# Kernel tuning notes

Hardware: AMD Instinct MI355X
Metric: run time of the kernel (lower is better)

The kernel has to match this reference:

```python
import jax, jax.numpy as jnp
import numpy as np

EPS = 1e-5
H = 1024  # hidden_size
IN = 1024  # input_size
B = 4096


def _layer_norm(x, gamma, beta):
    mu = jnp.mean(x, axis=-1, keepdims=True)
    var = jnp.mean(jnp.square(x - mu), axis=-1, keepdims=True)
    return (x - mu) * jax.lax.rsqrt(var + EPS) * gamma + beta


def setup_inputs() -> dict:
    key = jax.random.key(0)
    ks = jax.random.split(key, 8)
    s_h = 1.0 / np.sqrt(H)
    s_x = 1.0 / np.sqrt(IN)
    return {
        "x": jax.random.normal(ks[0], (B, IN), dtype=jnp.float32),
        "h": jax.random.normal(ks[1], (B, H), dtype=jnp.float32),
        "c": jax.random.normal(ks[2], (B, H), dtype=jnp.float32),
        # hidden_lin: Linear(H, 4H) with bias; input_lin: Linear(IN, 4H) no bias
        "W_h": jax.random.uniform(ks[3], (H, 4 * H), jnp.float32, -s_h, s_h),
        "b_h": jax.random.uniform(ks[4], (4 * H,), jnp.float32, -s_h, s_h),
        "W_x": jax.random.uniform(ks[5], (IN, 4 * H), jnp.float32, -s_x, s_x),
        # 4 gate LayerNorms stacked [4,H], plus LayerNorm for c
        "ln_g": jnp.ones((4, H), jnp.float32),
        "ln_b": jnp.zeros((4, H), jnp.float32),
        "lnc_g": jnp.ones((H,), jnp.float32),
        "lnc_b": jnp.zeros((H,), jnp.float32),
    }


def reference(x, h, c, W_h, b_h, W_x, ln_g, ln_b, lnc_g, lnc_b):
    # ifgo = hidden_lin(h) + input_lin(x) : [B, 4H]
    ifgo = h @ W_h + b_h + x @ W_x
    ifgo = ifgo.reshape(x.shape[0], 4, H)  # [B, 4, H]
    ifgo = _layer_norm(ifgo, ln_g, ln_b)   # per-gate LayerNorm over last dim
    i, f, g, o = ifgo[:, 0], ifgo[:, 1], ifgo[:, 2], ifgo[:, 3]
    c_next = jax.nn.sigmoid(f) * c + jax.nn.sigmoid(i) * jnp.tanh(g)
    h_next = jax.nn.sigmoid(o) * jnp.tanh(_layer_norm(c_next, lnc_g, lnc_b))
    return (h_next, c_next)
```

## Files before the change

### kernel.cpp

```cpp
#include <hip/hip_runtime.h>

typedef short bf16x8 __attribute__((ext_vector_type(8)));
typedef unsigned short u16x8 __attribute__((ext_vector_type(8)));
typedef float f32x4  __attribute__((ext_vector_type(4)));

__device__ __forceinline__ float bf2f(unsigned short u) {
  union { unsigned int i; float f; } x; x.i = ((unsigned int)u) << 16; return x.f;
}
__device__ __forceinline__ unsigned short f2bf(float f) {
  union { float f; unsigned int i; } x; x.f = f;
  unsigned int r = x.i + 0x7fffu + ((x.i >> 16) & 1u);
  return (unsigned short)(r >> 16);
}
__device__ __forceinline__ float sigm(float v) { return 1.f / (1.f + __expf(-v)); }
__device__ __forceinline__ float tanh_(float v) { return 1.f - 2.f / (__expf(2.f * v) + 1.f); }
__device__ __forceinline__ int is_fp32(const void* lng) {
  return ((*(const unsigned int*)lng) & 0xFFFFu) == 0u;
}

#define AS1 __attribute__((address_space(1)))
#define AS3 __attribute__((address_space(3)))

__global__ __launch_bounds__(256) void prep_kernel(
    const void* __restrict__ h, const void* __restrict__ x,
    const void* __restrict__ Wh, const void* __restrict__ Wx,
    const void* __restrict__ lng,
    unsigned short* __restrict__ Ap, unsigned short* __restrict__ Wt)
{
  __shared__ __align__(16) unsigned short tkn[64][64];
  const int fp = is_fp32(lng);
  if (blockIdx.x < 4096) {
    const int row = blockIdx.x;
    const int col = threadIdx.x * 8;
    const void* src; int sc;
    if (col < 1024) { src = h; sc = col; } else { src = x; sc = col - 1024; }
    u16x8 o;
    if (fp) {
      const float* s = (const float*)src + (size_t)row * 1024 + sc;
      float4 a = *(const float4*)s;
      float4 b = *(const float4*)(s + 4);
      o[0] = f2bf(a.x); o[1] = f2bf(a.y); o[2] = f2bf(a.z); o[3] = f2bf(a.w);
      o[4] = f2bf(b.x); o[5] = f2bf(b.y); o[6] = f2bf(b.z); o[7] = f2bf(b.w);
    } else {
      o = *(const u16x8*)((const unsigned short*)src + (size_t)row * 1024 + sc);
    }
    *(u16x8*)(Ap + (size_t)row * 2048 + col) = o;
  } else {
    const int bid = blockIdx.x - 4096;
    const int n0 = (bid & 63) * 64;
    const int k0 = (bid >> 6) * 64;
    const int t = threadIdx.x;
    const void* src; int krow;
    if (k0 < 1024) { src = Wh; krow = k0; } else { src = Wx; krow = k0 - 1024; }
    if (fp) {
#pragma unroll
      for (int i = 0; i < 4; ++i) {
        const int k  = (t >> 4) + i * 16;
        const int n4 = (t & 15) * 4;
        float4 w = *(const float4*)((const float*)src + (size_t)(krow + k) * 4096 + n0 + n4);
        ushort4 u; u.x = f2bf(w.x); u.y = f2bf(w.y); u.z = f2bf(w.z); u.w = f2bf(w.w);
        *(ushort4*)&tkn[k][n4] = u;
      }
    } else {
#pragma unroll
      for (int i = 0; i < 2; ++i) {
        const int k  = (t >> 3) + i * 32;
        const int n8 = (t & 7) * 8;
        *(u16x8*)&tkn[k][n8] =
            *(const u16x8*)((const unsigned short*)src + (size_t)(krow + k) * 4096 + n0 + n8);
      }
    }
    __syncthreads();
#pragma unroll
    for (int i = 0; i < 2; ++i) {
      const int n  = (t >> 3) + i * 32;
      const int k8 = (t & 7) * 8;
      u16x8 o;
#pragma unroll
      for (int j = 0; j < 8; ++j) o[j] = tkn[k8 + j][n];
      *(u16x8*)(Wt + (size_t)(n0 + n) * 2048 + k0 + k8) = o;
    }
  }
}


#define BAR()   __builtin_amdgcn_s_barrier()
#define VMW(N)  { asm volatile("s_waitcnt vmcnt(" #N ")" ::: "memory"); }

#define LOAD_A(DB, MH)                                                         \
  { const unsigned short* _ba = &As[DB][(MH)*128 + wr*64 + fr][0];             \
    _Pragma("unroll") for (int mi = 0; mi < 4; ++mi)                           \
      _Pragma("unroll") for (int kh = 0; kh < 2; ++kh)                         \
        a[mi][kh] = *(const bf16x8*)(_ba + mi*1024 + ((kh*4 + fq) ^ xk) * 8); }

#define LOAD_B(DB, NH, BT)                                                     \
  { const unsigned short* _bb = &Bs[DB][(NH)*128 + wc*32 + fr][0];             \
    _Pragma("unroll") for (int ni = 0; ni < 2; ++ni)                           \
      _Pragma("unroll") for (int kh = 0; kh < 2; ++kh)                         \
        (BT)[ni][kh] = *(const bf16x8*)(_bb + ni*1024 + ((kh*4 + fq) ^ xk) * 8); }

#define MFMA16(MH, NH, BT)                                                     \
  { __builtin_amdgcn_s_setprio(1);                                             \
    _Pragma("unroll") for (int kh = 0; kh < 2; ++kh)                           \
      _Pragma("unroll") for (int mi = 0; mi < 4; ++mi)                         \
        _Pragma("unroll") for (int ni = 0; ni < 2; ++ni)                       \
          acc[MH][mi][NH][ni] = __builtin_amdgcn_mfma_f32_16x16x32_bf16(       \
              a[mi][kh], (BT)[ni][kh], acc[MH][mi][NH][ni], 0, 0, 0);          \
    __builtin_amdgcn_s_setprio(0); }

#define STAGE(G, LDS, ROW0, H, KT)                                             \
  { _Pragma("unroll") for (int l = 0; l < 2; ++l) {                            \
      const int _idx = l * 512 + tid;                                          \
      const int _r = _idx >> 3;                                                \
      const int _sg = (_idx & 7) ^ (_r & 7);                                   \
      const unsigned short* _src = (G) + (size_t)((ROW0) + (H)*128 + _r) * 2048\
                                   + ((KT) << 6) + _sg * 8;                    \
      __builtin_amdgcn_global_load_lds((const AS1 void*)_src,                  \
          (AS3 void*)(&(LDS)[0][0] + (H)*8192 + (l*512 + wave*64)*8), 16, 0, 0);\
  } }

__global__ __launch_bounds__(512, 2) void gemm_kernel(
    const unsigned short* __restrict__ Ap,
    const unsigned short* __restrict__ Wt,
    unsigned short* __restrict__ Cout)
{
  __shared__ __align__(16) unsigned short As[2][256][64];
  __shared__ __align__(16) unsigned short Bs[2][256][64];

  const int bid = blockIdx.x;
  const int swz = (bid & 7) * 32 + (bid >> 3);
  const int bm = swz >> 4, bn = swz & 15;
  const int arow = bm * 256, brow = bn * 256;

  const int tid  = threadIdx.x;
  const int wave = tid >> 6, lane = tid & 63;
  const int wr = wave >> 2, wc = wave & 3;
  const int fr = lane & 15, fq = lane >> 4;
  const int xk = fr & 7;

  f32x4 acc[2][4][2][2] = {};
  bf16x8 a[4][2], bA[2][2], bB[2][2];

  STAGE(Wt, Bs[0], brow, 0, 0);
  STAGE(Ap, As[0], arow, 0, 0);
  STAGE(Wt, Bs[0], brow, 1, 0);
  STAGE(Ap, As[0], arow, 1, 0);
  STAGE(Wt, Bs[1], brow, 0, 1);
  STAGE(Ap, As[1], arow, 0, 1);
  VMW(4);
  BAR();
  LOAD_B(0, 0, bA)

#pragma unroll 1
  for (int it = 0; it < 16; ++it) {
    const int t1 = (2 * it + 1) & 31;
    const int t2 = (2 * it + 2) & 31;
    const int t3 = (2 * it + 3) & 31;

    VMW(8);
    LOAD_A(0, 0)
    STAGE(Wt, Bs[1], brow, 1, t1);
    BAR();
    MFMA16(0, 0, bA);
    BAR();
    VMW(8);
    LOAD_B(0, 1, bB)
    STAGE(Ap, As[1], arow, 1, t1);
    BAR();
    MFMA16(0, 1, bB);
    BAR();
    VMW(8);
    LOAD_A(0, 1)
    STAGE(Wt, Bs[0], brow, 0, t2);
    BAR();
    MFMA16(1, 1, bB);
    BAR();
    VMW(8);
    LOAD_B(1, 0, bB)
    STAGE(Ap, As[0], arow, 0, t2);
    BAR();
    MFMA16(1, 0, bA);
    BAR();
    VMW(8);
    LOAD_A(1, 0)
    STAGE(Wt, Bs[0], brow, 1, t2);
    BAR();
    MFMA16(0, 0, bB);
    BAR();
    VMW(8);
    LOAD_B(1, 1, bA)
    STAGE(Ap, As[0], arow, 1, t2);
    BAR();
    MFMA16(0, 1, bA);
    BAR();
    VMW(8);
    LOAD_A(1, 1)
    STAGE(Wt, Bs[1], brow, 0, t3);
    BAR();
    MFMA16(1, 1, bA);
    BAR();
    VMW(8);
    LOAD_B(0, 0, bA)
    STAGE(Ap, As[1], arow, 0, t3);
    BAR();
    MFMA16(1, 0, bB);
    BAR();
  }
  VMW(0);

  unsigned short* Cb = Cout + (size_t)arow * 4096 + brow;
#pragma unroll
  for (int mh = 0; mh < 2; ++mh)
#pragma unroll
    for (int mi = 0; mi < 4; ++mi)
#pragma unroll
      for (int nh = 0; nh < 2; ++nh)
#pragma unroll
        for (int ni = 0; ni < 2; ++ni) {
          const int row = mh * 128 + wr * 64 + mi * 16 + fq * 4;
          const int col = nh * 128 + wc * 32 + ni * 16 + fr;
#pragma unroll
          for (int r = 0; r < 4; ++r)
            Cb[(size_t)(row + r) * 4096 + col] = f2bf(acc[mh][mi][nh][ni][r]);
        }
}

__device__ __forceinline__ float4 load4(const void* p, size_t idx, int fp) {
  if (fp) return *(const float4*)((const float*)p + idx);
  ushort4 u = *(const ushort4*)((const unsigned short*)p + idx);
  return make_float4(bf2f(u.x), bf2f(u.y), bf2f(u.z), bf2f(u.w));
}
__device__ __forceinline__ void store4(void* p, size_t idx, int fp,
                                       float a, float b, float c, float d) {
  if (fp) {
    *(float4*)((float*)p + idx) = make_float4(a, b, c, d);
  } else {
    ushort4 u; u.x = f2bf(a); u.y = f2bf(b); u.z = f2bf(c); u.w = f2bf(d);
    *(ushort4*)((unsigned short*)p + idx) = u;
  }
}

__global__ __launch_bounds__(256) void ln_lstm_kernel(
    const unsigned short* __restrict__ parts,
    const void* __restrict__ c,
    const void* __restrict__ bh,
    const void* __restrict__ ln_g,
    const void* __restrict__ ln_b,
    const void* __restrict__ lnc_g,
    const void* __restrict__ lnc_b,
    void* __restrict__ out)
{
  const int b = blockIdx.x;
  const int t = threadIdx.x;
  const int lane = t & 63, wave = t >> 6;
  const int fp = is_fp32(lnc_g);
  const unsigned short* P0 = parts + (size_t)b * 4096;

  __shared__ float sred[4][8];

  float v[4][4];
  float red[8];
#pragma unroll
  for (int q = 0; q < 4; ++q) {
    ushort4 p0 = *(const ushort4*)(P0 + q * 1024 + t * 4);
    float4 b4 = load4(bh, q * 1024 + t * 4, fp);
    v[q][0] = bf2f(p0.x) + b4.x;
    v[q][1] = bf2f(p0.y) + b4.y;
    v[q][2] = bf2f(p0.z) + b4.z;
    v[q][3] = bf2f(p0.w) + b4.w;
    red[q * 2]     = v[q][0] + v[q][1] + v[q][2] + v[q][3];
    red[q * 2 + 1] = v[q][0]*v[q][0] + v[q][1]*v[q][1] + v[q][2]*v[q][2] + v[q][3]*v[q][3];
  }
#pragma unroll
  for (int j = 0; j < 8; ++j) {
    float s = red[j];
#pragma unroll
    for (int off = 32; off > 0; off >>= 1) s += __shfl_down(s, off, 64);
    if (lane == 0) sred[wave][j] = s;
  }
  __syncthreads();
  float mu[4], rs[4];
#pragma unroll
  for (int q = 0; q < 4; ++q) {
    float s  = sred[0][2*q]   + sred[1][2*q]   + sred[2][2*q]   + sred[3][2*q];
    float sq = sred[0][2*q+1] + sred[1][2*q+1] + sred[2][2*q+1] + sred[3][2*q+1];
    mu[q] = s * (1.f / 1024.f);
    float var = sq * (1.f / 1024.f) - mu[q] * mu[q];
    rs[q] = rsqrtf(var + 1e-5f);
  }

  float4 gI = load4(ln_g, 0 * 1024 + t * 4, fp), bI = load4(ln_b, 0 * 1024 + t * 4, fp);
  float4 gF = load4(ln_g, 1 * 1024 + t * 4, fp), bF = load4(ln_b, 1 * 1024 + t * 4, fp);
  float4 gG = load4(ln_g, 2 * 1024 + t * 4, fp), bG = load4(ln_b, 2 * 1024 + t * 4, fp);
  float4 gO = load4(ln_g, 3 * 1024 + t * 4, fp), bO = load4(ln_b, 3 * 1024 + t * 4, fp);
  float gg[4][4] = { {gI.x,gI.y,gI.z,gI.w}, {gF.x,gF.y,gF.z,gF.w},
                     {gG.x,gG.y,gG.z,gG.w}, {gO.x,gO.y,gO.z,gO.w} };
  float gb[4][4] = { {bI.x,bI.y,bI.z,bI.w}, {bF.x,bF.y,bF.z,bF.w},
                     {bG.x,bG.y,bG.z,bG.w}, {bO.x,bO.y,bO.z,bO.w} };

  float4 c4 = load4(c, (size_t)b * 1024 + t * 4, fp);
  float cin[4] = { c4.x, c4.y, c4.z, c4.w };

  float cn[4], osg[4];
  float csum = 0.f, csq = 0.f;
#pragma unroll
  for (int e = 0; e < 4; ++e) {
    float iv = (v[0][e] - mu[0]) * rs[0] * gg[0][e] + gb[0][e];
    float fv = (v[1][e] - mu[1]) * rs[1] * gg[1][e] + gb[1][e];
    float gv = (v[2][e] - mu[2]) * rs[2] * gg[2][e] + gb[2][e];
    float ov = (v[3][e] - mu[3]) * rs[3] * gg[3][e] + gb[3][e];
    float cne = sigm(fv) * cin[e] + sigm(iv) * tanh_(gv);
    cn[e] = cne; csum += cne; csq += cne * cne;
    osg[e] = sigm(ov);
  }
  store4(out, (size_t)4096 * 1024 + (size_t)b * 1024 + t * 4, fp, cn[0], cn[1], cn[2], cn[3]);

  __syncthreads();
  {
    float s0 = csum, s1 = csq;
#pragma unroll
    for (int off = 32; off > 0; off >>= 1) { s0 += __shfl_down(s0, off, 64); s1 += __shfl_down(s1, off, 64); }
    if (lane == 0) { sred[wave][0] = s0; sred[wave][1] = s1; }
  }
  __syncthreads();
  float cs   = sred[0][0] + sred[1][0] + sred[2][0] + sred[3][0];
  float csq2 = sred[0][1] + sred[1][1] + sred[2][1] + sred[3][1];
  float mu_c = cs * (1.f / 1024.f);
  float var_c = csq2 * (1.f / 1024.f) - mu_c * mu_c;
  float rs_c = rsqrtf(var_c + 1e-5f);

  float4 cg4 = load4(lnc_g, t * 4, fp);
  float4 cb4 = load4(lnc_b, t * 4, fp);

  float hn[4];
  float cgv[4] = { cg4.x, cg4.y, cg4.z, cg4.w };
  float cbv[4] = { cb4.x, cb4.y, cb4.z, cb4.w };
#pragma unroll
  for (int e = 0; e < 4; ++e)
    hn[e] = osg[e] * tanh_((cn[e] - mu_c) * rs_c * cgv[e] + cbv[e]);
  store4(out, (size_t)b * 1024 + t * 4, fp, hn[0], hn[1], hn[2], hn[3]);
}

extern "C" void kernel_launch(void* const* d_in, const int* in_sizes, int n_in,
                              void* d_out, int out_size, void* d_ws, size_t ws_size,
                              hipStream_t stream) {
  const void* x    = d_in[0];
  const void* h    = d_in[1];
  const void* c    = d_in[2];
  const void* Wh   = d_in[3];
  const void* bh   = d_in[4];
  const void* Wx   = d_in[5];
  const void* lng  = d_in[6];
  const void* lnb  = d_in[7];
  const void* lncg = d_in[8];
  const void* lncb = d_in[9];

  char* ws = (char*)d_ws;
  unsigned short* parts = (unsigned short*)ws;
  unsigned short* Wt    = (unsigned short*)(ws + (size_t)64 * 1024 * 1024);
  unsigned short* Ap    = (unsigned short*)(ws + (size_t)80 * 1024 * 1024);

  prep_kernel<<<6144, 256, 0, stream>>>(h, x, Wh, Wx, lng, Ap, Wt);
  gemm_kernel<<<256, 512, 0, stream>>>(Ap, Wt, parts);
  ln_lstm_kernel<<<4096, 256, 0, stream>>>(parts, c, bh, lng, lnb, lncg, lncb, d_out);
}
```

Baseline: 219.9 us.

## Deepen GEMM LDS prefetch pipeline and process four rows per LN-LSTM block

The GEMM main loop now prefetches a full k-tile ahead, staging both halves of the next buffer in the prologue. It waits on vmcnt only twice per half-iteration instead of before every sub-step, with an explicit lgkmcnt wait before the barriers that flip buffers. This aims to hide global-load latency better and cut wait stalls, at the risk of subtle read/write races in the double-buffered LDS. Separately, the LN-LSTM epilogue kernel handles four batch rows per block, loading the gamma, beta and bias vectors once and reusing them, which reduces block count and redundant parameter loads.

```diff
diff --git a/kernel.cpp b/kernel.cpp
--- a/kernel.cpp
+++ b/kernel.cpp
@@ -86,6 +86,7 @@
 
 #define BAR()   __builtin_amdgcn_s_barrier()
 #define VMW(N)  { asm volatile("s_waitcnt vmcnt(" #N ")" ::: "memory"); }
+#define LGKM0() { asm volatile("s_waitcnt lgkmcnt(0)" ::: "memory"); }
 
 #define LOAD_A(DB, MH)                                                         \
   { const unsigned short* _ba = &As[DB][(MH)*128 + wr*64 + fr][0];             \
@@ -147,63 +148,61 @@
   STAGE(Ap, As[0], arow, 1, 0);
   STAGE(Wt, Bs[1], brow, 0, 1);
   STAGE(Ap, As[1], arow, 0, 1);
-  VMW(4);
+  STAGE(Wt, Bs[1], brow, 1, 1);
+  STAGE(Ap, As[1], arow, 1, 1);
+  VMW(8);
   BAR();
   LOAD_B(0, 0, bA)
+  LGKM0();
 
 #pragma unroll 1
   for (int it = 0; it < 16; ++it) {
-    const int t1 = (2 * it + 1) & 31;
     const int t2 = (2 * it + 2) & 31;
     const int t3 = (2 * it + 3) & 31;
 
-    VMW(8);
     LOAD_A(0, 0)
-    STAGE(Wt, Bs[1], brow, 1, t1);
+    STAGE(Wt, Bs[0], brow, 0, t2);
     BAR();
     MFMA16(0, 0, bA);
     BAR();
-    VMW(8);
     LOAD_B(0, 1, bB)
-    STAGE(Ap, As[1], arow, 1, t1);
+    STAGE(Ap, As[0], arow, 0, t2);
     BAR();
     MFMA16(0, 1, bB);
     BAR();
-    VMW(8);
     LOAD_A(0, 1)
-    STAGE(Wt, Bs[0], brow, 0, t2);
+    STAGE(Wt, Bs[0], brow, 1, t2);
     BAR();
     MFMA16(1, 1, bB);
     BAR();
-    VMW(8);
+    VMW(6);
     LOAD_B(1, 0, bB)
-    STAGE(Ap, As[0], arow, 0, t2);
+    STAGE(Ap, As[0], arow, 1, t2);
     BAR();
     MFMA16(1, 0, bA);
-    BAR();
-    VMW(8);
+    LGKM0();
+    BAR();
     LOAD_A(1, 0)
-    STAGE(Wt, Bs[0], brow, 1, t2);
+    STAGE(Wt, Bs[1], brow, 0, t3);
     BAR();
     MFMA16(0, 0, bB);
     BAR();
-    VMW(8);
     LOAD_B(1, 1, bA)
-    STAGE(Ap, As[0], arow, 1, t2);
+    STAGE(Ap, As[1], arow, 0, t3);
     BAR();
     MFMA16(0, 1, bA);
     BAR();
-    VMW(8);
     LOAD_A(1, 1)
-    STAGE(Wt, Bs[1], brow, 0, t3);
+    STAGE(Wt, Bs[1], brow, 1, t3);
     BAR();
     MFMA16(1, 1, bA);
     BAR();
-    VMW(8);
+    VMW(6);
     LOAD_B(0, 0, bA)
-    STAGE(Ap, As[1], arow, 0, t3);
+    STAGE(Ap, As[1], arow, 1, t3);
     BAR();
     MFMA16(1, 0, bB);
+    LGKM0();
     BAR();
   }
   VMW(0);
@@ -250,95 +249,101 @@
     const void* __restrict__ lnc_b,
     void* __restrict__ out)
 {
-  const int b = blockIdx.x;
   const int t = threadIdx.x;
   const int lane = t & 63, wave = t >> 6;
   const int fp = is_fp32(lnc_g);
-  const unsigned short* P0 = parts + (size_t)b * 4096;
 
   __shared__ float sred[4][8];
 
-  float v[4][4];
-  float red[8];
+  float4 bias4[4];
+#pragma unroll
+  for (int q = 0; q < 4; ++q) bias4[q] = load4(bh, q * 1024 + t * 4, fp);
+  float gg[4][4], gb[4][4];
 #pragma unroll
   for (int q = 0; q < 4; ++q) {
-    ushort4 p0 = *(const ushort4*)(P0 + q * 1024 + t * 4);
-    float4 b4 = load4(bh, q * 1024 + t * 4, fp);
-    v[q][0] = bf2f(p0.x) + b4.x;
-    v[q][1] = bf2f(p0.y) + b4.y;
-    v[q][2] = bf2f(p0.z) + b4.z;
-    v[q][3] = bf2f(p0.w) + b4.w;
-    red[q * 2]     = v[q][0] + v[q][1] + v[q][2] + v[q][3];
-    red[q * 2 + 1] = v[q][0]*v[q][0] + v[q][1]*v[q][1] + v[q][2]*v[q][2] + v[q][3]*v[q][3];
-  }
-#pragma unroll
-  for (int j = 0; j < 8; ++j) {
-    float s = red[j];
-#pragma unroll
-    for (int off = 32; off > 0; off >>= 1) s += __shfl_down(s, off, 64);
-    if (lane == 0) sred[wave][j] = s;
-  }
-  __syncthreads();
-  float mu[4], rs[4];
-#pragma unroll
-  for (int q = 0; q < 4; ++q) {
-    float s  = sred[0][2*q]   + sred[1][2*q]   + sred[2][2*q]   + sred[3][2*q];
-    float sq = sred[0][2*q+1] + sred[1][2*q+1] + sred[2][2*q+1] + sred[3][2*q+1];
-    mu[q] = s * (1.f / 1024.f);
-    float var = sq * (1.f / 1024.f) - mu[q] * mu[q];
-    rs[q] = rsqrtf(var + 1e-5f);
-  }
-
-  float4 gI = load4(ln_g, 0 * 1024 + t * 4, fp), bI = load4(ln_b, 0 * 1024 + t * 4, fp);
-  float4 gF = load4(ln_g, 1 * 1024 + t * 4, fp), bF = load4(ln_b, 1 * 1024 + t * 4, fp);
-  float4 gG = load4(ln_g, 2 * 1024 + t * 4, fp), bG = load4(ln_b, 2 * 1024 + t * 4, fp);
-  float4 gO = load4(ln_g, 3 * 1024 + t * 4, fp), bO = load4(ln_b, 3 * 1024 + t * 4, fp);
-  float gg[4][4] = { {gI.x,gI.y,gI.z,gI.w}, {gF.x,gF.y,gF.z,gF.w},
-                     {gG.x,gG.y,gG.z,gG.w}, {gO.x,gO.y,gO.z,gO.w} };
-  float gb[4][4] = { {bI.x,bI.y,bI.z,bI.w}, {bF.x,bF.y,bF.z,bF.w},
-                     {bG.x,bG.y,bG.z,bG.w}, {bO.x,bO.y,bO.z,bO.w} };
-
-  float4 c4 = load4(c, (size_t)b * 1024 + t * 4, fp);
-  float cin[4] = { c4.x, c4.y, c4.z, c4.w };
-
-  float cn[4], osg[4];
-  float csum = 0.f, csq = 0.f;
-#pragma unroll
-  for (int e = 0; e < 4; ++e) {
-    float iv = (v[0][e] - mu[0]) * rs[0] * gg[0][e] + gb[0][e];
-    float fv = (v[1][e] - mu[1]) * rs[1] * gg[1][e] + gb[1][e];
-    float gv = (v[2][e] - mu[2]) * rs[2] * gg[2][e] + gb[2][e];
-    float ov = (v[3][e] - mu[3]) * rs[3] * gg[3][e] + gb[3][e];
-    float cne = sigm(fv) * cin[e] + sigm(iv) * tanh_(gv);
-    cn[e] = cne; csum += cne; csq += cne * cne;
-    osg[e] = sigm(ov);
-  }
-  store4(out, (size_t)4096 * 1024 + (size_t)b * 1024 + t * 4, fp, cn[0], cn[1], cn[2], cn[3]);
-
-  __syncthreads();
-  {
-    float s0 = csum, s1 = csq;
-#pragma unroll
-    for (int off = 32; off > 0; off >>= 1) { s0 += __shfl_down(s0, off, 64); s1 += __shfl_down(s1, off, 64); }
-    if (lane == 0) { sred[wave][0] = s0; sred[wave][1] = s1; }
-  }
-  __syncthreads();
-  float cs   = sred[0][0] + sred[1][0] + sred[2][0] + sred[3][0];
-  float csq2 = sred[0][1] + sred[1][1] + sred[2][1] + sred[3][1];
-  float mu_c = cs * (1.f / 1024.f);
-  float var_c = csq2 * (1.f / 1024.f) - mu_c * mu_c;
-  float rs_c = rsqrtf(var_c + 1e-5f);
-
+    float4 g4 = load4(ln_g, q * 1024 + t * 4, fp);
+    float4 b4 = load4(ln_b, q * 1024 + t * 4, fp);
+    gg[q][0] = g4.x; gg[q][1] = g4.y; gg[q][2] = g4.z; gg[q][3] = g4.w;
+    gb[q][0] = b4.x; gb[q][1] = b4.y; gb[q][2] = b4.z; gb[q][3] = b4.w;
+  }
   float4 cg4 = load4(lnc_g, t * 4, fp);
   float4 cb4 = load4(lnc_b, t * 4, fp);
-
-  float hn[4];
   float cgv[4] = { cg4.x, cg4.y, cg4.z, cg4.w };
   float cbv[4] = { cb4.x, cb4.y, cb4.z, cb4.w };
-#pragma unroll
-  for (int e = 0; e < 4; ++e)
-    hn[e] = osg[e] * tanh_((cn[e] - mu_c) * rs_c * cgv[e] + cbv[e]);
-  store4(out, (size_t)b * 1024 + t * 4, fp, hn[0], hn[1], hn[2], hn[3]);
+
+#pragma unroll 1
+  for (int r = 0; r < 4; ++r) {
+    const int b = blockIdx.x * 4 + r;
+    const unsigned short* P0 = parts + (size_t)b * 4096;
+    __syncthreads();
+
+    float v[4][4];
+    float red[8];
+#pragma unroll
+    for (int q = 0; q < 4; ++q) {
+      ushort4 p0 = *(const ushort4*)(P0 + q * 1024 + t * 4);
+      v[q][0] = bf2f(p0.x) + bias4[q].x;
+      v[q][1] = bf2f(p0.y) + bias4[q].y;
+      v[q][2] = bf2f(p0.z) + bias4[q].z;
+      v[q][3] = bf2f(p0.w) + bias4[q].w;
+      red[q * 2]     = v[q][0] + v[q][1] + v[q][2] + v[q][3];
+      red[q * 2 + 1] = v[q][0]*v[q][0] + v[q][1]*v[q][1] + v[q][2]*v[q][2] + v[q][3]*v[q][3];
+    }
+#pragma unroll
+    for (int j = 0; j < 8; ++j) {
+      float s = red[j];
+#pragma unroll
+      for (int off = 32; off > 0; off >>= 1) s += __shfl_down(s, off, 64);
+      if (lane == 0) sred[wave][j] = s;
+    }
+    __syncthreads();
+    float mu[4], rs[4];
+#pragma unroll
+    for (int q = 0; q < 4; ++q) {
+      float s  = sred[0][2*q]   + sred[1][2*q]   + sred[2][2*q]   + sred[3][2*q];
+      float sq = sred[0][2*q+1] + sred[1][2*q+1] + sred[2][2*q+1] + sred[3][2*q+1];
+      mu[q] = s * (1.f / 1024.f);
+      float var = sq * (1.f / 1024.f) - mu[q] * mu[q];
+      rs[q] = rsqrtf(var + 1e-5f);
+    }
+
+    float4 c4 = load4(c, (size_t)b * 1024 + t * 4, fp);
+    float cin[4] = { c4.x, c4.y, c4.z, c4.w };
+
+    float cn[4], osg[4];
+    float csum = 0.f, csq = 0.f;
+#pragma unroll
+    for (int e = 0; e < 4; ++e) {
+      float iv = (v[0][e] - mu[0]) * rs[0] * gg[0][e] + gb[0][e];
+      float fv = (v[1][e] - mu[1]) * rs[1] * gg[1][e] + gb[1][e];
+      float gv = (v[2][e] - mu[2]) * rs[2] * gg[2][e] + gb[2][e];
+      float ov = (v[3][e] - mu[3]) * rs[3] * gg[3][e] + gb[3][e];
+      float cne = sigm(fv) * cin[e] + sigm(iv) * tanh_(gv);
+      cn[e] = cne; csum += cne; csq += cne * cne;
+      osg[e] = sigm(ov);
+    }
+    store4(out, (size_t)4096 * 1024 + (size_t)b * 1024 + t * 4, fp, cn[0], cn[1], cn[2], cn[3]);
+
+    __syncthreads();
+    {
+      float s0 = csum, s1 = csq;
+#pragma unroll
+      for (int off = 32; off > 0; off >>= 1) { s0 += __shfl_down(s0, off, 64); s1 += __shfl_down(s1, off, 64); }
+      if (lane == 0) { sred[wave][0] = s0; sred[wave][1] = s1; }
+    }
+    __syncthreads();
+    float cs   = sred[0][0] + sred[1][0] + sred[2][0] + sred[3][0];
+    float csq2 = sred[0][1] + sred[1][1] + sred[2][1] + sred[3][1];
+    float mu_c = cs * (1.f / 1024.f);
+    float var_c = csq2 * (1.f / 1024.f) - mu_c * mu_c;
+    float rs_c = rsqrtf(var_c + 1e-5f);
+
+    float hn[4];
+#pragma unroll
+    for (int e = 0; e < 4; ++e)
+      hn[e] = osg[e] * tanh_((cn[e] - mu_c) * rs_c * cgv[e] + cbv[e]);
+    store4(out, (size_t)b * 1024 + t * 4, fp, hn[0], hn[1], hn[2], hn[3]);
+  }
 }
 
 extern "C" void kernel_launch(void* const* d_in, const int* in_sizes, int n_in,
@@ -362,5 +367,5 @@
 
   prep_kernel<<<6144, 256, 0, stream>>>(h, x, Wh, Wx, lng, Ap, Wt);
   gemm_kernel<<<256, 512, 0, stream>>>(Ap, Wt, parts);
-  ln_lstm_kernel<<<4096, 256, 0, stream>>>(parts, c, bh, lng, lnb, lncg, lncb, d_out);
-}
+  ln_lstm_kernel<<<1024, 256, 0, stream>>>(parts, c, bh, lng, lnb, lncg, lncb, d_out);
+}
```

New measurement: 217.9 us. No clear change (-0.9%).
